# Performance work log

Hardware: AMD Instinct MI355X
Metric: run time of the kernel (lower is better)

The kernel has to match this reference:

```python
import jax, jax.numpy as jnp
import numpy as np

B, L, HID = 32, 1, 3072
H, KV, D = 16, 8, 256
S = 2048
SCALE = D ** -0.5


def setup_inputs() -> dict:
    key = jax.random.key(0)
    ks = jax.random.split(key, 10)
    return {
        "hidden_states": jax.random.normal(ks[0], (B, L, HID), jnp.float32),
        "freqs_cos": jax.random.normal(ks[1], (B, L, D // 2), jnp.float32),
        "freqs_sin": jax.random.normal(ks[2], (B, L, D // 2), jnp.float32),
        "mask": jnp.zeros((B, 1, 1, S), jnp.float32),
        "cache_k": jax.random.normal(ks[3], (B, KV, S, D), jnp.float32),
        "cache_v": jax.random.normal(ks[4], (B, KV, S, D), jnp.float32),
        "wq": jax.random.normal(ks[5], (HID, H * D), jnp.float32) * 0.02,
        "wk": jax.random.normal(ks[6], (HID, KV * D), jnp.float32) * 0.02,
        "wv": jax.random.normal(ks[7], (HID, KV * D), jnp.float32) * 0.02,
        "wo": jax.random.normal(ks[8], (H * D, HID), jnp.float32) * 0.02,
        "pos": 2047,
    }


def _rope(x, cos, sin):
    # x: [B, L, nh, D]; cos/sin: [B, L, D/2]. Split-half complex rotation:
    # pairs are (x[..., i], x[..., i + D/2]), matching torch chunk+view_as_complex.
    half = x.shape[-1] // 2
    xr, xi = x[..., :half], x[..., half:]
    c = cos[:, :, None, :]
    s = sin[:, :, None, :]
    return jnp.concatenate([xr * c - xi * s, xr * s + xi * c], axis=-1)


def reference(hidden_states, freqs_cos, freqs_sin, mask, cache_k, cache_v,
              wq, wk, wv, wo, pos):
    G = H // KV  # queries per kv head
    xq = (hidden_states @ wq).reshape(B, L, H, D)
    xk = (hidden_states @ wk).reshape(B, L, KV, D)
    xv = (hidden_states @ wv).reshape(B, L, KV, D)

    xq = _rope(xq, freqs_cos, freqs_sin)
    xk = _rope(xk, freqs_cos, freqs_sin)

    # [B, heads, L, D]
    xq = xq.transpose(0, 2, 1, 3)
    xk = xk.transpose(0, 2, 1, 3)
    xv = xv.transpose(0, 2, 1, 3)

    # insert current step into the KV cache at static position `pos`
    cache_k = cache_k.at[:, :, pos:pos + L, :].set(xk)
    cache_v = cache_v.at[:, :, pos:pos + L, :].set(xv)

    # GQA attention over the full cache without materializing repeated KV
    q = xq.reshape(B, KV, G, L, D)
    scores = jnp.einsum('bkgqd,bksd->bkgqs', q, cache_k) * SCALE
    scores = scores + mask[:, :, None]  # [B,1,1,1,S] broadcast
    probs = jax.nn.softmax(scores, axis=-1)
    out = jnp.einsum('bkgqs,bksd->bkgqd', probs, cache_v)

    out = out.reshape(B, H, L, D).transpose(0, 2, 1, 3).reshape(B, L, H * D)
    return out @ wo
```

## Files before the change

kernel.cpp:

```cpp
#include <hip/hip_runtime.h>
#include <hip/hip_bf16.h>


#define SCALE_ 0.0625f

#define OFF_XQKV (8u*32u*8192u)
#define OFF_ATTN (OFF_XQKV + 32u*8192u)
#define OFF_PO   (OFF_ATTN + 32u*4096u)
#define OFF_ML   (1048576u)

__device__ inline void fma4(float4& a, float s, const float4& w) {
  a.x = fmaf(s, w.x, a.x); a.y = fmaf(s, w.y, a.y);
  a.z = fmaf(s, w.z, a.z); a.w = fmaf(s, w.w, a.w);
}
__device__ inline float dot4(const float4& a, const float4& b) {
  return a.x * b.x + a.y * b.y + a.z * b.z + a.w * b.w;
}
__device__ inline void scale_fma4(float4& a, float sc, float p, const float4& v) {
  a.x = fmaf(a.x, sc, p * v.x); a.y = fmaf(a.y, sc, p * v.y);
  a.z = fmaf(a.z, sc, p * v.z); a.w = fmaf(a.w, sc, p * v.w);
}

__global__ __launch_bounds__(512) void qkv_partial_kernel(
    const float* __restrict__ x, const float* __restrict__ wq,
    const float* __restrict__ wk, const float* __restrict__ wv,
    float* __restrict__ pqkv) {
  const int lane = threadIdx.x & 63;
  const int bg   = threadIdx.x >> 6;
  const int ctile = blockIdx.x & 31;
  const int kc    = blockIdx.x >> 5;
  const int n = ctile * 256 + lane * 4;

  const float* w; int stride, nn;
  if (n < 4096)      { w = wq; stride = 4096; nn = n; }
  else if (n < 6144) { w = wk; stride = 2048; nn = n - 4096; }
  else               { w = wv; stride = 2048; nn = n - 6144; }

  const float* wb = w + (size_t)(kc * 384) * stride + nn;
  const float* xb = x + (size_t)(bg * 4) * 3072 + kc * 384;

  float4 acc[4];
#pragma unroll
  for (int j = 0; j < 4; ++j) acc[j] = make_float4(0.f, 0.f, 0.f, 0.f);

  for (int k = 0; k < 384; k += 4) {
    float4 w0 = *(const float4*)(wb + (size_t)(k + 0) * stride);
    float4 w1 = *(const float4*)(wb + (size_t)(k + 1) * stride);
    float4 w2 = *(const float4*)(wb + (size_t)(k + 2) * stride);
    float4 w3 = *(const float4*)(wb + (size_t)(k + 3) * stride);
#pragma unroll
    for (int j = 0; j < 4; ++j) {
      float4 xv = *(const float4*)(xb + j * 3072 + k);
      fma4(acc[j], xv.x, w0);
      fma4(acc[j], xv.y, w1);
      fma4(acc[j], xv.z, w2);
      fma4(acc[j], xv.w, w3);
    }
  }
#pragma unroll
  for (int j = 0; j < 4; ++j) {
    *(float4*)(pqkv + ((size_t)kc * 32 + bg * 4 + j) * 8192 + n) = acc[j];
  }
}

__global__ __launch_bounds__(256) void reduce_rope_kernel(
    const float* __restrict__ pqkv, const float* __restrict__ fcos,
    const float* __restrict__ fsin, float* __restrict__ xqkv) {
  const int w = blockIdx.x * 256 + threadIdx.x;
  const int b = w / 5120;
  const int r = w - b * 5120;
  const float* pb = pqkv + (size_t)b * 8192;
  float* ob = xqkv + (size_t)b * 8192;

  if (r < 3072) {
    int n1, d;
    const bool isq = (r < 2048);
    if (isq) { int h = r >> 7; d = r & 127; n1 = h * 256 + d; }
    else     { int idx = r - 2048; int kvh = idx >> 7; d = idx & 127;
               n1 = 4096 + kvh * 256 + d; }
    const int n2 = n1 + 128;
    float xr = 0.f, xi = 0.f;
#pragma unroll
    for (int kc = 0; kc < 8; ++kc) {
      xr += pb[(size_t)kc * 262144 + n1];
      xi += pb[(size_t)kc * 262144 + n2];
    }
    const float c = fcos[b * 128 + d];
    const float s = fsin[b * 128 + d];
    float o1 = xr * c - xi * s;
    float o2 = xr * s + xi * c;
    if (isq) { o1 *= SCALE_; o2 *= SCALE_; }
    ob[n1] = o1;
    ob[n2] = o2;
  } else {
    const int nn = 6144 + (r - 3072);
    float v = 0.f;
#pragma unroll
    for (int kc = 0; kc < 8; ++kc) v += pb[(size_t)kc * 262144 + nn];
    ob[nn] = v;
  }
}

__global__ __launch_bounds__(256) void attn_chunk_kernel(
    const float* __restrict__ xqkv, const float* __restrict__ cache_k,
    const float* __restrict__ cache_v, const float* __restrict__ mask,
    const int* __restrict__ posp, float* __restrict__ opart,
    float* __restrict__ ml) {
  __shared__ float accbuf[8][512];
  __shared__ float mred[8][4];

  const int tid = threadIdx.x, lane = tid & 63, wv = tid >> 6;
  const int sub = lane & 31;
  const int stream = wv * 2 + (lane >> 5);
  const int c  = blockIdx.x & 7;
  const int kv = (blockIdx.x >> 3) & 7;
  const int b  = blockIdx.x >> 6;
  const int pos = posp[0];
  const int s0 = c * 256;
  const int dbase = sub * 8;

  const float* xb = xqkv + (size_t)b * 8192;
  const float* knew = xb + 4096 + kv * 256;
  const float* vnew = xb + 6144 + kv * 256;
  const size_t base = ((size_t)b * 8 + kv) * 2048 * 256;
  const float* kbase = cache_k + base;
  const float* vbase = cache_v + base;
  const float* mrow = mask + (size_t)b * 2048;

  const float4 qa0 = *(const float4*)(xb + (kv * 2 + 0) * 256 + dbase);
  const float4 qa1 = *(const float4*)(xb + (kv * 2 + 0) * 256 + dbase + 4);
  const float4 qb0 = *(const float4*)(xb + (kv * 2 + 1) * 256 + dbase);
  const float4 qb1 = *(const float4*)(xb + (kv * 2 + 1) * 256 + dbase + 4);

  float m0 = -3.4e38f, l0 = 0.f, m1 = -3.4e38f, l1 = 0.f;
  float4 a00 = make_float4(0.f, 0.f, 0.f, 0.f);
  float4 a01 = make_float4(0.f, 0.f, 0.f, 0.f);
  float4 a10 = make_float4(0.f, 0.f, 0.f, 0.f);
  float4 a11 = make_float4(0.f, 0.f, 0.f, 0.f);

  int sA = s0 + stream;
  int sB = sA + 8;
  const float* krA = (sA == pos) ? knew : (kbase + (size_t)sA * 256);
  const float* vrA = (sA == pos) ? vnew : (vbase + (size_t)sA * 256);
  const float* krB = (sB == pos) ? knew : (kbase + (size_t)sB * 256);
  const float* vrB = (sB == pos) ? vnew : (vbase + (size_t)sB * 256);
  float4 kA0 = *(const float4*)(krA + dbase);
  float4 kA1 = *(const float4*)(krA + dbase + 4);
  float4 vA0 = *(const float4*)(vrA + dbase);
  float4 vA1 = *(const float4*)(vrA + dbase + 4);
  float mkA = mrow[sA];
  float4 kB0 = *(const float4*)(krB + dbase);
  float4 kB1 = *(const float4*)(krB + dbase + 4);
  float4 vB0 = *(const float4*)(vrB + dbase);
  float4 vB1 = *(const float4*)(vrB + dbase + 4);
  float mkB = mrow[sB];

  for (int i = 0; i < 32; i += 2) {
    {
      float d0 = dot4(qa0, kA0) + dot4(qa1, kA1);
      float d1 = dot4(qb0, kA0) + dot4(qb1, kA1);
      const int ipf = (i + 2 < 32) ? (i + 2) : 31;
      const int sn = s0 + stream + 8 * ipf;
      const float* krn = (sn == pos) ? knew : (kbase + (size_t)sn * 256);
      const float* vrn = (sn == pos) ? vnew : (vbase + (size_t)sn * 256);
      kA0 = *(const float4*)(krn + dbase);
      kA1 = *(const float4*)(krn + dbase + 4);
      const float mkn = mrow[sn];
#pragma unroll
      for (int off = 16; off > 0; off >>= 1) {
        d0 += __shfl_xor(d0, off);
        d1 += __shfl_xor(d1, off);
      }
      d0 += mkA; d1 += mkA;
      const float nm0 = fmaxf(m0, d0);
      const float al0 = __expf(m0 - nm0);
      const float p0  = __expf(d0 - nm0);
      m0 = nm0; l0 = fmaf(l0, al0, p0);
      scale_fma4(a00, al0, p0, vA0);
      scale_fma4(a01, al0, p0, vA1);
      const float nm1 = fmaxf(m1, d1);
      const float al1 = __expf(m1 - nm1);
      const float p1  = __expf(d1 - nm1);
      m1 = nm1; l1 = fmaf(l1, al1, p1);
      scale_fma4(a10, al1, p1, vA0);
      scale_fma4(a11, al1, p1, vA1);
      vA0 = *(const float4*)(vrn + dbase);
      vA1 = *(const float4*)(vrn + dbase + 4);
      mkA = mkn;
    }
    {
      float d0 = dot4(qa0, kB0) + dot4(qa1, kB1);
      float d1 = dot4(qb0, kB0) + dot4(qb1, kB1);
      const int ipf = (i + 3 < 32) ? (i + 3) : 31;
      const int sn = s0 + stream + 8 * ipf;
      const float* krn = (sn == pos) ? knew : (kbase + (size_t)sn * 256);
      const float* vrn = (sn == pos) ? vnew : (vbase + (size_t)sn * 256);
      kB0 = *(const float4*)(krn + dbase);
      kB1 = *(const float4*)(krn + dbase + 4);
      const float mkn = mrow[sn];
#pragma unroll
      for (int off = 16; off > 0; off >>= 1) {
        d0 += __shfl_xor(d0, off);
        d1 += __shfl_xor(d1, off);
      }
      d0 += mkB; d1 += mkB;
      const float nm0 = fmaxf(m0, d0);
      const float al0 = __expf(m0 - nm0);
      const float p0  = __expf(d0 - nm0);
      m0 = nm0; l0 = fmaf(l0, al0, p0);
      scale_fma4(a00, al0, p0, vB0);
      scale_fma4(a01, al0, p0, vB1);
      const float nm1 = fmaxf(m1, d1);
      const float al1 = __expf(m1 - nm1);
      const float p1  = __expf(d1 - nm1);
      m1 = nm1; l1 = fmaf(l1, al1, p1);
      scale_fma4(a10, al1, p1, vB0);
      scale_fma4(a11, al1, p1, vB1);
      vB0 = *(const float4*)(vrn + dbase);
      vB1 = *(const float4*)(vrn + dbase + 4);
      mkB = mkn;
    }
  }

  if (sub == 0) {
    mred[stream][0] = m0; mred[stream][1] = l0;
    mred[stream][2] = m1; mred[stream][3] = l1;
  }
  __syncthreads();
  float M0 = -3.4e38f, M1 = -3.4e38f;
#pragma unroll
  for (int t = 0; t < 8; ++t) {
    M0 = fmaxf(M0, mred[t][0]);
    M1 = fmaxf(M1, mred[t][2]);
  }
  const float sc0 = __expf(m0 - M0);
  const float sc1 = __expf(m1 - M1);
  float* ab = &accbuf[stream][0];
  ab[dbase + 0] = a00.x * sc0; ab[dbase + 1] = a00.y * sc0;
  ab[dbase + 2] = a00.z * sc0; ab[dbase + 3] = a00.w * sc0;
  ab[dbase + 4] = a01.x * sc0; ab[dbase + 5] = a01.y * sc0;
  ab[dbase + 6] = a01.z * sc0; ab[dbase + 7] = a01.w * sc0;
  ab[256 + dbase + 0] = a10.x * sc1; ab[256 + dbase + 1] = a10.y * sc1;
  ab[256 + dbase + 2] = a10.z * sc1; ab[256 + dbase + 3] = a10.w * sc1;
  ab[256 + dbase + 4] = a11.x * sc1; ab[256 + dbase + 5] = a11.y * sc1;
  ab[256 + dbase + 6] = a11.z * sc1; ab[256 + dbase + 7] = a11.w * sc1;
  __syncthreads();

  if (tid == 0) {
    float L0 = 0.f, L1 = 0.f;
#pragma unroll
    for (int t = 0; t < 8; ++t) {
      L0 = fmaf(mred[t][1], __expf(mred[t][0] - M0), L0);
      L1 = fmaf(mred[t][3], __expf(mred[t][2] - M1), L1);
    }
    float2* mlp = (float2*)ml;
    const int mlbase = (((b * 8 + kv) * 8) + c) * 2;
    mlp[mlbase + 0] = make_float2(M0, L0);
    mlp[mlbase + 1] = make_float2(M1, L1);
  }

  const size_t obase = (size_t)((b * 8 + kv) * 8 + c) * 512;
  for (int t = tid; t < 512; t += 256) {
    float sum = 0.f;
#pragma unroll
    for (int st = 0; st < 8; ++st) sum += accbuf[st][t];
    opart[obase + t] = sum;
  }
}

__global__ __launch_bounds__(512) void oproj_fused_kernel(
    const float* __restrict__ opart, const float* __restrict__ ml,
    const float* __restrict__ wo, float* __restrict__ po) {
  __shared__ float xs[32][256];

  const int t = threadIdx.x;
  const int ctile = blockIdx.x % 12;
  const int kc    = blockIdx.x / 12;
  const int kvh = kc >> 1, g = kc & 1;

  {
    const int b = t >> 4;
    const int d0 = (t & 15) * 16;
    const int kvb = b * 8 + kvh;
    const float2* mlp = (const float2*)ml;
    float2 mls[8];
    float M = -3.4e38f;
#pragma unroll
    for (int c = 0; c < 8; ++c) {
      mls[c] = mlp[(kvb * 8 + c) * 2 + g];
      M = fmaxf(M, mls[c].x);
    }
    float L = 0.f;
    float4 O[4];
#pragma unroll
    for (int q = 0; q < 4; ++q) O[q] = make_float4(0.f, 0.f, 0.f, 0.f);
#pragma unroll
    for (int c = 0; c < 8; ++c) {
      const float wc = __expf(mls[c].x - M);
      L = fmaf(mls[c].y, wc, L);
      const float4* src =
          (const float4*)(opart + (size_t)(kvb * 8 + c) * 512 + g * 256 + d0);
      fma4(O[0], wc, src[0]); fma4(O[1], wc, src[1]);
      fma4(O[2], wc, src[2]); fma4(O[3], wc, src[3]);
    }
    const float invL = 1.f / L;
    float4* dst = (float4*)(&xs[b][d0]);
#pragma unroll
    for (int q = 0; q < 4; ++q) {
      dst[q] = make_float4(O[q].x * invL, O[q].y * invL,
                           O[q].z * invL, O[q].w * invL);
    }
  }
  __syncthreads();

  const int lane = t & 63;
  const int bg   = t >> 6;
  const int n = ctile * 256 + lane * 4;
  const float* wb = wo + (size_t)(kc * 256) * 3072 + n;

  float4 acc[4];
#pragma unroll
  for (int j = 0; j < 4; ++j) acc[j] = make_float4(0.f, 0.f, 0.f, 0.f);

  for (int k = 0; k < 256; k += 4) {
    float4 w0 = *(const float4*)(wb + (size_t)(k + 0) * 3072);
    float4 w1 = *(const float4*)(wb + (size_t)(k + 1) * 3072);
    float4 w2 = *(const float4*)(wb + (size_t)(k + 2) * 3072);
    float4 w3 = *(const float4*)(wb + (size_t)(k + 3) * 3072);
#pragma unroll
    for (int j = 0; j < 4; ++j) {
      const float* xr = &xs[bg * 4 + j][k];
      fma4(acc[j], xr[0], w0);
      fma4(acc[j], xr[1], w1);
      fma4(acc[j], xr[2], w2);
      fma4(acc[j], xr[3], w3);
    }
  }
#pragma unroll
  for (int j = 0; j < 4; ++j) {
    *(float4*)(po + ((size_t)kc * 32 + bg * 4 + j) * 3072 + n) = acc[j];
  }
}

__global__ __launch_bounds__(256) void finalize_kernel(
    const float* __restrict__ po, float* __restrict__ out) {
  const int i = blockIdx.x * 256 + threadIdx.x;
  const float4* p = (const float4*)po;
  float4 acc = make_float4(0.f, 0.f, 0.f, 0.f);
#pragma unroll
  for (int kc = 0; kc < 16; ++kc) {
    const float4 v = p[(size_t)kc * 24576 + i];
    acc.x += v.x; acc.y += v.y; acc.z += v.z; acc.w += v.w;
  }
  ((float4*)out)[i] = acc;
}

extern "C" void kernel_launch(void* const* d_in, const int* in_sizes, int n_in,
                              void* d_out, int out_size, void* d_ws, size_t ws_size,
                              hipStream_t stream) {
  (void)in_sizes; (void)n_in; (void)out_size; (void)ws_size;
  const float* x    = (const float*)d_in[0];
  const float* fcos = (const float*)d_in[1];
  const float* fsin = (const float*)d_in[2];
  const float* mask = (const float*)d_in[3];
  const float* ck   = (const float*)d_in[4];
  const float* cv   = (const float*)d_in[5];
  const float* wq   = (const float*)d_in[6];
  const float* wk   = (const float*)d_in[7];
  const float* wv   = (const float*)d_in[8];
  const float* wo   = (const float*)d_in[9];
  const int*   pos  = (const int*)d_in[10];

  float* ws    = (float*)d_ws;
  float* pqkv  = ws;
  float* opart = ws;
  float* ml    = ws + OFF_ML;
  float* xqkv  = ws + OFF_XQKV;
  float* po    = ws + OFF_PO;
  float* out   = (float*)d_out;

  qkv_partial_kernel<<<256, 512, 0, stream>>>(x, wq, wk, wv, pqkv);
  reduce_rope_kernel<<<640, 256, 0, stream>>>(pqkv, fcos, fsin, xqkv);
  attn_chunk_kernel<<<2048, 256, 0, stream>>>(xqkv, ck, cv, mask, pos, opart, ml);
  oproj_fused_kernel<<<192, 512, 0, stream>>>(opart, ml, wo, po);
  finalize_kernel<<<96, 256, 0, stream>>>(po, out);
}
```

Baseline: 324.5 us.

## Stage x in LDS, double-buffer weight loads, vectorize reduce, retile o-proj

The QKV partial GEMM now stages the activation slice in shared memory and double-buffers its weight-row loads in registers, so the next loads are issued while the current FMAs run. The reduce/RoPE kernel handles four elements per thread with float4 loads and stores and launches a quarter as many blocks. The output projection is retiled to 256-thread blocks over 128 columns, which doubles the block count, and it gets the same double-buffered weight loads. All of this targets latency in the weight-bandwidth-bound GEMV stages, at the cost of more registers and shared memory per block.

```diff
diff --git a/kernel.cpp b/kernel.cpp
--- a/kernel.cpp
+++ b/kernel.cpp
@@ -25,38 +25,64 @@
     const float* __restrict__ x, const float* __restrict__ wq,
     const float* __restrict__ wk, const float* __restrict__ wv,
     float* __restrict__ pqkv) {
+  __shared__ float xls[32][384];
+
   const int lane = threadIdx.x & 63;
   const int bg   = threadIdx.x >> 6;
   const int ctile = blockIdx.x & 31;
   const int kc    = blockIdx.x >> 5;
   const int n = ctile * 256 + lane * 4;
 
+  for (int i = threadIdx.x; i < 3072; i += 512) {
+    const int b = i / 96;
+    const int r = i - b * 96;
+    *(float4*)(&xls[b][r * 4]) =
+        *(const float4*)(x + (size_t)b * 3072 + kc * 384 + r * 4);
+  }
+
   const float* w; int stride, nn;
   if (n < 4096)      { w = wq; stride = 4096; nn = n; }
   else if (n < 6144) { w = wk; stride = 2048; nn = n - 4096; }
   else               { w = wv; stride = 2048; nn = n - 6144; }
-
   const float* wb = w + (size_t)(kc * 384) * stride + nn;
-  const float* xb = x + (size_t)(bg * 4) * 3072 + kc * 384;
 
   float4 acc[4];
 #pragma unroll
   for (int j = 0; j < 4; ++j) acc[j] = make_float4(0.f, 0.f, 0.f, 0.f);
 
-  for (int k = 0; k < 384; k += 4) {
-    float4 w0 = *(const float4*)(wb + (size_t)(k + 0) * stride);
-    float4 w1 = *(const float4*)(wb + (size_t)(k + 1) * stride);
-    float4 w2 = *(const float4*)(wb + (size_t)(k + 2) * stride);
-    float4 w3 = *(const float4*)(wb + (size_t)(k + 3) * stride);
-#pragma unroll
-    for (int j = 0; j < 4; ++j) {
-      float4 xv = *(const float4*)(xb + j * 3072 + k);
-      fma4(acc[j], xv.x, w0);
-      fma4(acc[j], xv.y, w1);
-      fma4(acc[j], xv.z, w2);
-      fma4(acc[j], xv.w, w3);
-    }
-  }
+  __syncthreads();
+
+  float4 wA[4], wB[4];
+#define LDW(S, KK)                                                   \
+  {                                                                  \
+    S[0] = *(const float4*)(wb + (size_t)((KK) + 0) * stride);       \
+    S[1] = *(const float4*)(wb + (size_t)((KK) + 1) * stride);       \
+    S[2] = *(const float4*)(wb + (size_t)((KK) + 2) * stride);       \
+    S[3] = *(const float4*)(wb + (size_t)((KK) + 3) * stride);       \
+  }
+#define CMP(S, KK)                                                   \
+  {                                                                  \
+    _Pragma("unroll")                                                \
+    for (int j = 0; j < 4; ++j) {                                    \
+      const float4 xv = *(const float4*)(&xls[bg * 4 + j][(KK)]);    \
+      fma4(acc[j], xv.x, S[0]);                                      \
+      fma4(acc[j], xv.y, S[1]);                                      \
+      fma4(acc[j], xv.z, S[2]);                                      \
+      fma4(acc[j], xv.w, S[3]);                                      \
+    }                                                                \
+  }
+
+  LDW(wA, 0);
+  for (int k = 0; k < 384; k += 8) {
+    LDW(wB, k + 4);
+    CMP(wA, k);
+    const int kn = (k + 8 < 384) ? (k + 8) : 0;
+    LDW(wA, kn);
+    CMP(wB, k + 4);
+  }
+#undef LDW
+#undef CMP
+
 #pragma unroll
   for (int j = 0; j < 4; ++j) {
     *(float4*)(pqkv + ((size_t)kc * 32 + bg * 4 + j) * 8192 + n) = acc[j];
@@ -67,37 +93,49 @@
     const float* __restrict__ pqkv, const float* __restrict__ fcos,
     const float* __restrict__ fsin, float* __restrict__ xqkv) {
   const int w = blockIdx.x * 256 + threadIdx.x;
-  const int b = w / 5120;
-  const int r = w - b * 5120;
+  const int b = w / 1280;
+  const int r = w - b * 1280;
   const float* pb = pqkv + (size_t)b * 8192;
   float* ob = xqkv + (size_t)b * 8192;
 
-  if (r < 3072) {
+  if (r < 768) {
     int n1, d;
-    const bool isq = (r < 2048);
-    if (isq) { int h = r >> 7; d = r & 127; n1 = h * 256 + d; }
-    else     { int idx = r - 2048; int kvh = idx >> 7; d = idx & 127;
+    const bool isq = (r < 512);
+    if (isq) { const int h = r >> 5; d = (r & 31) * 4; n1 = h * 256 + d; }
+    else     { const int p = r - 512; const int kvh = p >> 5; d = (p & 31) * 4;
                n1 = 4096 + kvh * 256 + d; }
     const int n2 = n1 + 128;
-    float xr = 0.f, xi = 0.f;
+    float4 xr = make_float4(0.f, 0.f, 0.f, 0.f);
+    float4 xi = make_float4(0.f, 0.f, 0.f, 0.f);
 #pragma unroll
     for (int kc = 0; kc < 8; ++kc) {
-      xr += pb[(size_t)kc * 262144 + n1];
-      xi += pb[(size_t)kc * 262144 + n2];
-    }
-    const float c = fcos[b * 128 + d];
-    const float s = fsin[b * 128 + d];
-    float o1 = xr * c - xi * s;
-    float o2 = xr * s + xi * c;
-    if (isq) { o1 *= SCALE_; o2 *= SCALE_; }
-    ob[n1] = o1;
-    ob[n2] = o2;
+      const float4 a = *(const float4*)(pb + (size_t)kc * 262144 + n1);
+      const float4 c = *(const float4*)(pb + (size_t)kc * 262144 + n2);
+      xr.x += a.x; xr.y += a.y; xr.z += a.z; xr.w += a.w;
+      xi.x += c.x; xi.y += c.y; xi.z += c.z; xi.w += c.w;
+    }
+    const float4 c = *(const float4*)(fcos + b * 128 + d);
+    const float4 s = *(const float4*)(fsin + b * 128 + d);
+    float4 o1, o2;
+    o1.x = xr.x * c.x - xi.x * s.x;  o2.x = xr.x * s.x + xi.x * c.x;
+    o1.y = xr.y * c.y - xi.y * s.y;  o2.y = xr.y * s.y + xi.y * c.y;
+    o1.z = xr.z * c.z - xi.z * s.z;  o2.z = xr.z * s.z + xi.z * c.z;
+    o1.w = xr.w * c.w - xi.w * s.w;  o2.w = xr.w * s.w + xi.w * c.w;
+    if (isq) {
+      o1.x *= SCALE_; o1.y *= SCALE_; o1.z *= SCALE_; o1.w *= SCALE_;
+      o2.x *= SCALE_; o2.y *= SCALE_; o2.z *= SCALE_; o2.w *= SCALE_;
+    }
+    *(float4*)(ob + n1) = o1;
+    *(float4*)(ob + n2) = o2;
   } else {
-    const int nn = 6144 + (r - 3072);
-    float v = 0.f;
-#pragma unroll
-    for (int kc = 0; kc < 8; ++kc) v += pb[(size_t)kc * 262144 + nn];
-    ob[nn] = v;
+    const int nn = 6144 + (r - 768) * 4;
+    float4 v = make_float4(0.f, 0.f, 0.f, 0.f);
+#pragma unroll
+    for (int kc = 0; kc < 8; ++kc) {
+      const float4 a = *(const float4*)(pb + (size_t)kc * 262144 + nn);
+      v.x += a.x; v.y += a.y; v.z += a.z; v.w += a.w;
+    }
+    *(float4*)(ob + nn) = v;
   }
 }
 
@@ -268,19 +306,19 @@
   }
 }
 
-__global__ __launch_bounds__(512) void oproj_fused_kernel(
+__global__ __launch_bounds__(256) void oproj_fused_kernel(
     const float* __restrict__ opart, const float* __restrict__ ml,
     const float* __restrict__ wo, float* __restrict__ po) {
   __shared__ float xs[32][256];
 
   const int t = threadIdx.x;
-  const int ctile = blockIdx.x % 12;
-  const int kc    = blockIdx.x / 12;
+  const int ctile = blockIdx.x % 24;
+  const int kc    = blockIdx.x / 24;
   const int kvh = kc >> 1, g = kc & 1;
 
   {
-    const int b = t >> 4;
-    const int d0 = (t & 15) * 16;
+    const int b = t >> 3;
+    const int d0 = (t & 7) * 32;
     const int kvb = b * 8 + kvh;
     const float2* mlp = (const float2*)ml;
     float2 mls[8];
@@ -291,54 +329,71 @@
       M = fmaxf(M, mls[c].x);
     }
     float L = 0.f;
-    float4 O[4];
-#pragma unroll
-    for (int q = 0; q < 4; ++q) O[q] = make_float4(0.f, 0.f, 0.f, 0.f);
+    float4 O[8];
+#pragma unroll
+    for (int q = 0; q < 8; ++q) O[q] = make_float4(0.f, 0.f, 0.f, 0.f);
 #pragma unroll
     for (int c = 0; c < 8; ++c) {
       const float wc = __expf(mls[c].x - M);
       L = fmaf(mls[c].y, wc, L);
       const float4* src =
           (const float4*)(opart + (size_t)(kvb * 8 + c) * 512 + g * 256 + d0);
-      fma4(O[0], wc, src[0]); fma4(O[1], wc, src[1]);
-      fma4(O[2], wc, src[2]); fma4(O[3], wc, src[3]);
+#pragma unroll
+      for (int q = 0; q < 8; ++q) fma4(O[q], wc, src[q]);
     }
     const float invL = 1.f / L;
     float4* dst = (float4*)(&xs[b][d0]);
 #pragma unroll
-    for (int q = 0; q < 4; ++q) {
+    for (int q = 0; q < 8; ++q) {
       dst[q] = make_float4(O[q].x * invL, O[q].y * invL,
                            O[q].z * invL, O[q].w * invL);
     }
   }
   __syncthreads();
 
-  const int lane = t & 63;
-  const int bg   = t >> 6;
-  const int n = ctile * 256 + lane * 4;
+  const int lane = t & 31;
+  const int half = t >> 5;
+  const int n = ctile * 128 + lane * 4;
   const float* wb = wo + (size_t)(kc * 256) * 3072 + n;
 
   float4 acc[4];
 #pragma unroll
   for (int j = 0; j < 4; ++j) acc[j] = make_float4(0.f, 0.f, 0.f, 0.f);
 
-  for (int k = 0; k < 256; k += 4) {
-    float4 w0 = *(const float4*)(wb + (size_t)(k + 0) * 3072);
-    float4 w1 = *(const float4*)(wb + (size_t)(k + 1) * 3072);
-    float4 w2 = *(const float4*)(wb + (size_t)(k + 2) * 3072);
-    float4 w3 = *(const float4*)(wb + (size_t)(k + 3) * 3072);
-#pragma unroll
-    for (int j = 0; j < 4; ++j) {
-      const float* xr = &xs[bg * 4 + j][k];
-      fma4(acc[j], xr[0], w0);
-      fma4(acc[j], xr[1], w1);
-      fma4(acc[j], xr[2], w2);
-      fma4(acc[j], xr[3], w3);
-    }
-  }
+  float4 wA[4], wB[4];
+#define LDW(S, KK)                                                 \
+  {                                                                \
+    S[0] = *(const float4*)(wb + (size_t)((KK) + 0) * 3072);       \
+    S[1] = *(const float4*)(wb + (size_t)((KK) + 1) * 3072);       \
+    S[2] = *(const float4*)(wb + (size_t)((KK) + 2) * 3072);       \
+    S[3] = *(const float4*)(wb + (size_t)((KK) + 3) * 3072);       \
+  }
+#define CMP(S, KK)                                                 \
+  {                                                                \
+    _Pragma("unroll")                                              \
+    for (int j = 0; j < 4; ++j) {                                  \
+      const float4 xv = *(const float4*)(&xs[half * 4 + j][(KK)]); \
+      fma4(acc[j], xv.x, S[0]);                                    \
+      fma4(acc[j], xv.y, S[1]);                                    \
+      fma4(acc[j], xv.z, S[2]);                                    \
+      fma4(acc[j], xv.w, S[3]);                                    \
+    }                                                              \
+  }
+
+  LDW(wA, 0);
+  for (int k = 0; k < 256; k += 8) {
+    LDW(wB, k + 4);
+    CMP(wA, k);
+    const int kn = (k + 8 < 256) ? (k + 8) : 0;
+    LDW(wA, kn);
+    CMP(wB, k + 4);
+  }
+#undef LDW
+#undef CMP
+
 #pragma unroll
   for (int j = 0; j < 4; ++j) {
-    *(float4*)(po + ((size_t)kc * 32 + bg * 4 + j) * 3072 + n) = acc[j];
+    *(float4*)(po + ((size_t)kc * 32 + half * 4 + j) * 3072 + n) = acc[j];
   }
 }
 
@@ -380,8 +435,8 @@
   float* out   = (float*)d_out;
 
   qkv_partial_kernel<<<256, 512, 0, stream>>>(x, wq, wk, wv, pqkv);
-  reduce_rope_kernel<<<640, 256, 0, stream>>>(pqkv, fcos, fsin, xqkv);
+  reduce_rope_kernel<<<160, 256, 0, stream>>>(pqkv, fcos, fsin, xqkv);
   attn_chunk_kernel<<<2048, 256, 0, stream>>>(xqkv, ck, cv, mask, pos, opart, ml);
-  oproj_fused_kernel<<<192, 512, 0, stream>>>(opart, ml, wo, po);
+  oproj_fused_kernel<<<384, 256, 0, stream>>>(opart, ml, wo, po);
   finalize_kernel<<<96, 256, 0, stream>>>(po, out);
 }
```

Result: no change. 328.5 us (+1.2%).
